# Optimization experiments

Hardware: AMD Instinct MI355X
Metric: run time of the kernel (lower is better)

Reference implementation:

```python
import jax, jax.numpy as jnp
import numpy as np

INF = 1.0e10


def _embed(x, W1, b1, W2, b2):
    # TemplateAngleEmbedder: Linear -> GELU -> Linear
    return jax.nn.gelu(x @ W1 + b1) @ W2 + b2


def setup_inputs() -> dict:
    key = jax.random.key(0)
    ks = jax.random.split(key, 12)
    B, N, K = 2, 768, 30
    d_pair, d_msa, relpos_k = 128, 256, 32
    num_bins = 2 * relpos_k + 1  # 65
    s = 0.02
    # valid rigid frames: random rotations via QR (det fixed to +1) + translations
    A = jax.random.normal(ks[0], (B, N, 3, 3), dtype=jnp.float32)
    Q, _ = jnp.linalg.qr(A)
    Q = Q * jnp.sign(jnp.linalg.det(Q))[..., None, None]
    t = jax.random.normal(ks[1], (B, N, 3), dtype=jnp.float32) * 10.0
    frames = (jnp.zeros((B, N, 4, 4), dtype=jnp.float32)
              .at[..., :3, :3].set(Q)
              .at[..., :3, 3].set(t)
              .at[..., 3, 3].set(1.0))
    residue_index = jnp.tile(jnp.arange(N, dtype=jnp.int32)[None], (B, 1))
    return {
        'tf': jax.random.normal(ks[2], (B, N, 1), dtype=jnp.float32),
        'residue_index': residue_index,
        'true_frame_tensor': frames,
        'seq_mask': jnp.ones((B, N), dtype=jnp.float32),
        'W_tf': jax.random.normal(ks[3], (1, d_msa), dtype=jnp.float32) * s,
        'b_tf': jnp.zeros((d_msa,), dtype=jnp.float32),
        'Wa1': jax.random.normal(ks[4], (5, d_pair), dtype=jnp.float32) * s,
        'ba1': jnp.zeros((d_pair,), dtype=jnp.float32),
        'Wa2': jax.random.normal(ks[5], (d_pair, d_pair), dtype=jnp.float32) * s,
        'ba2': jnp.zeros((d_pair,), dtype=jnp.float32),
        'Wd1': jax.random.normal(ks[6], (3, d_pair), dtype=jnp.float32) * s,
        'bd1': jnp.zeros((d_pair,), dtype=jnp.float32),
        'Wd2': jax.random.normal(ks[7], (d_pair, d_pair), dtype=jnp.float32) * s,
        'bd2': jnp.zeros((d_pair,), dtype=jnp.float32),
        'W_rp': jax.random.normal(ks[8], (num_bins, d_pair), dtype=jnp.float32) * s,
        'b_rp': jnp.zeros((d_pair,), dtype=jnp.float32),
        'topk': 30,
    }


def _pair_features(true_frame_tensor, residue_index, seq_mask, topk):
    # get_pair_info: pairwise dist + masked topk KNN + gather + frame decompose
    B, N = residue_index.shape
    R = true_frame_tensor[..., :3, :3]          # [B,N,3,3]
    t = true_frame_tensor[..., :3, 3]           # [B,N,3]
    xyz = t[:, None, :, :] - t[:, :, None, :]   # [B,i,j,3] = t_j - t_i
    dist = jnp.linalg.norm(xyz, axis=-1)        # [B,N,N]
    eye = jnp.eye(N, dtype=bool)[None]          # [1,N,N]
    smask = seq_mask.astype(bool)
    pair_mask = smask[:, None, :] & smask[:, :, None]
    rel = residue_index[:, None, :] - residue_index[:, :, None]
    connect = jnp.abs(rel) == 1
    d4topk = jnp.where(eye, INF, dist)
    d4topk = jnp.where(pair_mask, d4topk, INF)
    d4topk = jnp.where(connect, -INF, d4topk)
    _, idx = jax.lax.top_k(-d4topk, topk)       # k smallest -> [B,N,K]
    topk_dist = jnp.take_along_axis(dist, idx, axis=-1)          # [B,N,K]
    knn_mask = jnp.take_along_axis(pair_mask & ~eye, idx, axis=-1)
    # gather neighbor frames and decompose into frame i's local coordinates:
    # t_rel = R_i^T (t_j - t_i)
    bidx = jnp.arange(B)[:, None, None]
    tj = t[bidx, idx]                            # [B,N,K,3]
    t_rel = jnp.einsum('bnxy,bnkx->bnky', R, tj - t[:, :, None, :])
    d = topk_dist[..., None]
    direct_angle = jnp.where(d > 0, t_rel / jnp.where(d > 0, d, 1.0), 0.0)
    eye_g = jnp.take_along_axis(jnp.broadcast_to(eye, (B, N, N)), idx, axis=-1)
    conn_g = jnp.take_along_axis(connect, idx, axis=-1)
    f32 = topk_dist.dtype
    ang_in = jnp.concatenate([eye_g[..., None].astype(f32),
                              conn_g[..., None].astype(f32),
                              direct_angle], axis=-1)            # [B,N,K,5]
    dst_in = jnp.concatenate([eye_g[..., None].astype(f32),
                              conn_g[..., None].astype(f32),
                              topk_dist[..., None]], axis=-1)    # [B,N,K,3]
    return ang_in, dst_in, knn_mask


def reference(tf, residue_index, true_frame_tensor, seq_mask,
              W_tf, b_tf, Wa1, ba1, Wa2, ba2, Wd1, bd1, Wd2, bd2,
              W_rp, b_rp, topk):
    relpos_k = (W_rp.shape[0] - 1) // 2
    # pair info computed under no_grad in the original
    ang_in, dst_in, _ = jax.lax.stop_gradient(
        _pair_features(true_frame_tensor, residue_index, seq_mask, topk))
    # tf is replaced by ones in the original forward
    ones_tf = jnp.ones_like(tf[..., :1])
    s = ones_tf @ W_tf + b_tf                                   # [B,N,d_msa]
    pair_rep_angle = _embed(ang_in, Wa1, ba1, Wa2, ba2)         # [B,N,K,d_pair]
    pair_rep_dist = _embed(dst_in, Wd1, bd1, Wd2, bd2)          # [B,N,K,d_pair]
    # relpos embedding (use_chain_relative=False)
    rp = residue_index[:, :, None] - residue_index[:, None, :]
    rp = jnp.clip(rp, -relpos_k, relpos_k) + relpos_k
    oh = jax.nn.one_hot(rp, W_rp.shape[0], dtype=W_rp.dtype)    # [B,N,N,65]
    relpos_emb = oh @ W_rp + b_rp                               # [B,N,N,d_pair]
    return (s, pair_rep_angle, pair_rep_dist, relpos_emb)
```

## Files before the change

kernel.cpp:

```cpp
#include <hip/hip_runtime.h>

typedef unsigned short u16;
typedef unsigned int   u32;
typedef unsigned long long u64;

typedef __attribute__((ext_vector_type(8))) short  short8;
typedef __attribute__((ext_vector_type(4))) float  floatx4;

__device__ __forceinline__ u16 f2bf(float f) {
    u32 u = __float_as_uint(f);
    u32 r = (u + 0x7FFFu + ((u >> 16) & 1u)) >> 16;
    return (u16)r;
}
__device__ __forceinline__ float bfu2f(u16 u) {
    union { u32 i; float f; } v; v.i = ((u32)u) << 16; return v.f;
}

constexpr int N     = 768;
constexpr int TOPK  = 30;
constexpr long OFF_ANG = 393216;
constexpr long OFF_DST = 6291456;
constexpr long OFF_RP  = 12189696;

__device__ __forceinline__ float dist_f32(float dx, float dy, float dz) {
    float s = __fadd_rn(__fadd_rn(__fmul_rn(dx, dx), __fmul_rn(dy, dy)), __fmul_rn(dz, dz));
    return __fsqrt_rn(s);
}

__global__ __launch_bounds__(256) void topk_relpos_kernel(
    const float* __restrict__ frames, const int* __restrict__ resi,
    const float* __restrict__ smask, float* __restrict__ feat,
    const float* __restrict__ W_rp, const float* __restrict__ b_rp,
    float* __restrict__ out)
{
    __shared__ __align__(16) char smem_raw[65 * 128 * 4 + N * 4];
    int tid = threadIdx.x;

    if (blockIdx.x < 384) {
        float* s_t = (float*)smem_raw;
        float* s_m = s_t + N * 3;
        int*   s_r = (int*)(s_m + N);

        int r0  = blockIdx.x * 4;
        int b   = r0 / N;
        for (int j = tid; j < N; j += 256) {
            s_r[j] = resi[b * N + j];
            s_m[j] = smask[b * N + j];
            long fb = (long)(b * N + j) * 16;
            s_t[j * 3 + 0] = frames[fb + 0 * 4 + 3];
            s_t[j * 3 + 1] = frames[fb + 1 * 4 + 3];
            s_t[j * 3 + 2] = frames[fb + 2 * 4 + 3];
        }
        __syncthreads();

        int wave = tid >> 6, lane = tid & 63;
        int r = r0 + wave;
        int i = r - b * N;
        float ti0 = s_t[i * 3], ti1 = s_t[i * 3 + 1], ti2 = s_t[i * 3 + 2];
        float mi = s_m[i];
        int   ri = s_r[i];

        u64 keys[12];
#pragma unroll
        for (int c = 0; c < 12; c++) {
            int j = lane + 64 * c;
            float dx = __fadd_rn(s_t[j * 3 + 0], -ti0);
            float dy = __fadd_rn(s_t[j * 3 + 1], -ti1);
            float dz = __fadd_rn(s_t[j * 3 + 2], -ti2);
            float dist = dist_f32(dx, dy, dz);
            int rd = s_r[j] - ri;
            bool conn = (rd == 1) || (rd == -1);
            bool bad  = (j == i) || (mi == 0.f) || (s_m[j] == 0.f);
            float d4 = conn ? -1e10f : (bad ? 1e10f : dist);
            u32 u = __float_as_uint(d4);
            u32 su = (u >> 31) ? ~u : (u | 0x80000000u);
            keys[c] = ((u64)su << 32) | (u32)j;
        }

        int my_j = 0;
        for (int k = 0; k < TOPK; k++) {
            u64 m = keys[0];
#pragma unroll
            for (int c = 1; c < 12; c++) m = m < keys[c] ? m : keys[c];
#pragma unroll
            for (int off = 32; off >= 1; off >>= 1) {
                u32 lo = (u32)m, hi = (u32)(m >> 32);
                u32 lo2 = __shfl_xor(lo, off);
                u32 hi2 = __shfl_xor(hi, off);
                u64 o = ((u64)hi2 << 32) | lo2;
                m = m < o ? m : o;
            }
#pragma unroll
            for (int c = 0; c < 12; c++) keys[c] = (keys[c] == m) ? ~0ull : keys[c];
            if (lane == k) my_j = (int)(m & 0xffffffffu);
        }

        if (lane < TOPK) {
            int j = my_j;
            float dx = __fadd_rn(s_t[j * 3 + 0], -ti0);
            float dy = __fadd_rn(s_t[j * 3 + 1], -ti1);
            float dz = __fadd_rn(s_t[j * 3 + 2], -ti2);
            float dist = dist_f32(dx, dy, dz);
            long fb = (long)(b * N + i) * 16;
            float R00 = frames[fb + 0], R01 = frames[fb + 1], R02 = frames[fb + 2];
            float R10 = frames[fb + 4], R11 = frames[fb + 5], R12 = frames[fb + 6];
            float R20 = frames[fb + 8], R21 = frames[fb + 9], R22 = frames[fb + 10];
            float t0 = R00 * dx + R10 * dy + R20 * dz;
            float t1 = R01 * dx + R11 * dy + R21 * dz;
            float t2 = R02 * dx + R12 * dy + R22 * dz;
            float a0 = dist > 0.f ? t0 / dist : 0.f;
            float a1 = dist > 0.f ? t1 / dist : 0.f;
            float a2 = dist > 0.f ? t2 / dist : 0.f;
            int rd = s_r[j] - ri;
            float conn = ((rd == 1) || (rd == -1)) ? 1.f : 0.f;
            float eye  = (j == i) ? 1.f : 0.f;
            long base = ((long)r * TOPK + lane) * 8;
            feat[base + 0] = eye; feat[base + 1] = conn;
            feat[base + 2] = a0;  feat[base + 3] = a1; feat[base + 4] = a2;
            feat[base + 5] = eye; feat[base + 6] = conn; feat[base + 7] = dist;
        }
    } else {
        float* T   = (float*)smem_raw;
        int*   s_r = (int*)(T + 65 * 128);

        int blk = blockIdx.x - 384;
        int b   = blk >= 576;

        for (int e = tid; e < 65 * 128; e += 256) T[e] = W_rp[e] + b_rp[e & 127];
        for (int j = tid; j < N; j += 256) s_r[j] = resi[b * N + j];
        __syncthreads();

        long vbase   = (long)blk << 15;
        int  rowbase = (blk - b * 576) << 10;
        floatx4* dst = (floatx4*)(out + OFF_RP) + vbase;

#pragma unroll 4
        for (int it = 0; it < 128; ++it) {
            int lv  = (it << 8) + tid;
            unsigned lrow = (unsigned)(rowbase + (lv >> 5));
            int seg = lv & 31;
            unsigned i = lrow / 768u;
            unsigned j = lrow - i * 768u;
            int d = s_r[i] - s_r[j];
            d = d < -32 ? -32 : (d > 32 ? 32 : d);
            dst[lv] = ((const floatx4*)(T + (unsigned)(d + 32) * 128))[seg];
        }
    }
}

template<int NF, int FOFF>
__device__ __forceinline__ void embed_body(
    int blk, const float* __restrict__ feat,
    const float* __restrict__ W1, const float* __restrict__ b1,
    const float* __restrict__ W2, const float* __restrict__ b2,
    float* __restrict__ out,
    u16* s_w2h, u16* s_w2l, float* s_w1, float* s_b1, float* s_b2)
{
    int tid = threadIdx.x;
    for (int e = tid; e < 128 * 128; e += 256) {
        int kk = e >> 7, nn = e & 127;
        float w  = W2[e];
        u16 hi = f2bf(w);
        float lo = __fadd_rn(w, -bfu2f(hi));
        s_w2h[nn * 136 + kk] = hi;
        s_w2l[nn * 136 + kk] = f2bf(lo);
    }
    for (int e = tid; e < NF * 128; e += 256) s_w1[e] = W1[e];
    if (tid < 128) { s_b1[tid] = b1[tid]; s_b2[tid] = b2[tid]; }
    __syncthreads();

    int wave = tid >> 6, lane = tid & 63;
    int m = lane & 15, q = lane >> 4;
    int row0 = blk * 64 + wave * 16;
    int row  = row0 + m;

    float f[NF];
#pragma unroll
    for (int t = 0; t < NF; t++) f[t] = feat[(long)row * 8 + FOFF + t];

    floatx4 acc[8];
#pragma unroll
    for (int nt = 0; nt < 8; nt++) acc[nt] = (floatx4){0.f, 0.f, 0.f, 0.f};

#pragma unroll
    for (int s = 0; s < 4; s++) {
        short8 ahi, alo;
#pragma unroll
        for (int jj = 0; jj < 8; jj++) {
            int kk = 32 * s + 8 * q + jj;
            float h = s_b1[kk];
#pragma unroll
            for (int t = 0; t < NF; t++) h += f[t] * s_w1[t * 128 + kk];
            float u  = 0.7978845608028654f * (h + 0.044715f * h * h * h);
            float e2 = __expf(-2.f * fabsf(u));
            float th = (1.f - e2) / (1.f + e2);
            th = u < 0.f ? -th : th;
            float g = 0.5f * h * (1.f + th);
            u16 ghi = f2bf(g);
            float glo = __fadd_rn(g, -bfu2f(ghi));
            ahi[jj] = (short)ghi;
            alo[jj] = (short)f2bf(glo);
        }
#pragma unroll
        for (int nt = 0; nt < 8; nt++) {
            int boff = (nt * 16 + m) * 136 + 32 * s + 8 * q;
            short8 bh = *(const short8*)&s_w2h[boff];
            short8 bl = *(const short8*)&s_w2l[boff];
            acc[nt] = __builtin_amdgcn_mfma_f32_16x16x32_bf16(ahi, bh, acc[nt], 0, 0, 0);
            acc[nt] = __builtin_amdgcn_mfma_f32_16x16x32_bf16(alo, bh, acc[nt], 0, 0, 0);
            acc[nt] = __builtin_amdgcn_mfma_f32_16x16x32_bf16(ahi, bl, acc[nt], 0, 0, 0);
        }
    }

#pragma unroll
    for (int nt = 0; nt < 8; nt++) {
#pragma unroll
        for (int rg = 0; rg < 4; rg++) {
            int rr = row0 + q * 4 + rg;
            int cc = nt * 16 + m;
            out[(long)rr * 128 + cc] = acc[nt][rg] + s_b2[cc];
        }
    }
}

__global__ __launch_bounds__(256) void fused_embed_s_kernel(
    const float* __restrict__ feat,
    const float* __restrict__ Wa1, const float* __restrict__ ba1,
    const float* __restrict__ Wa2, const float* __restrict__ ba2,
    const float* __restrict__ Wd1, const float* __restrict__ bd1,
    const float* __restrict__ Wd2, const float* __restrict__ bd2,
    const float* __restrict__ W_tf, const float* __restrict__ b_tf,
    float* __restrict__ out)
{
    __shared__ __align__(16) u16 s_w2h[128 * 136];
    __shared__ __align__(16) u16 s_w2l[128 * 136];
    __shared__ float s_w1[5 * 128];
    __shared__ float s_b1[128];
    __shared__ float s_b2[128];
    unsigned bx = blockIdx.x;
    if (bx < 720) {
        embed_body<5, 0>(bx, feat, Wa1, ba1, Wa2, ba2, out + OFF_ANG,
                         s_w2h, s_w2l, s_w1, s_b1, s_b2);
    } else if (bx < 1440) {
        embed_body<3, 5>(bx - 720, feat, Wd1, bd1, Wd2, bd2, out + OFF_DST,
                         s_w2h, s_w2l, s_w1, s_b1, s_b2);
    } else {
        int gid = (bx - 1440) * 256 + threadIdx.x;
        int c0  = (gid * 4) & 255;
        floatx4 o;
        o.x = W_tf[c0 + 0] + b_tf[c0 + 0];
        o.y = W_tf[c0 + 1] + b_tf[c0 + 1];
        o.z = W_tf[c0 + 2] + b_tf[c0 + 2];
        o.w = W_tf[c0 + 3] + b_tf[c0 + 3];
        *((floatx4*)out + gid) = o;
    }
}

extern "C" void kernel_launch(void* const* d_in, const int* in_sizes, int n_in,
                              void* d_out, int out_size, void* d_ws, size_t ws_size,
                              hipStream_t stream) {
    const int*   resi   = (const int*)d_in[1];
    const float* frames = (const float*)d_in[2];
    const float* smask  = (const float*)d_in[3];
    const float* W_tf   = (const float*)d_in[4];
    const float* b_tf   = (const float*)d_in[5];
    const float* Wa1    = (const float*)d_in[6];
    const float* ba1    = (const float*)d_in[7];
    const float* Wa2    = (const float*)d_in[8];
    const float* ba2    = (const float*)d_in[9];
    const float* Wd1    = (const float*)d_in[10];
    const float* bd1    = (const float*)d_in[11];
    const float* Wd2    = (const float*)d_in[12];
    const float* bd2    = (const float*)d_in[13];
    const float* W_rp   = (const float*)d_in[14];
    const float* b_rp   = (const float*)d_in[15];
    float* out  = (float*)d_out;
    float* feat = (float*)d_ws;

    hipLaunchKernelGGL(topk_relpos_kernel, dim3(1536), dim3(256), 0, stream,
                       frames, resi, smask, feat, W_rp, b_rp, out);
    hipLaunchKernelGGL(fused_embed_s_kernel, dim3(1824), dim3(256), 0, stream,
                       feat, Wa1, ba1, Wa2, ba2, Wd1, bd1, Wd2, bd2,
                       W_tf, b_tf, out);
}
```

Baseline: 701.0 us.

## Split top-k into its own kernel and co-schedule relpos with embedding MLPs

The top-k feature kernel now runs alone with 384 blocks. The relpos broadcast moves into a second mega kernel next to the angle and distance embed MLPs, so the bandwidth-bound relpos writes can overlap with MFMA-bound embedding work instead of overlapping with top-k. Each embed block now handles three 64-row tiles, which amortizes the W2 bf16 hi/lo split into LDS across more rows, and W2 is read with float4 loads. The costs are a larger shared allocation (about 73 KB) for every block in the mega kernel, which may cut occupancy for the relpos blocks, and a top-k kernel with few blocks that may underfill the GPU.

Result: slower. 747.5 us (+6.6%).

```diff
diff --git a/kernel.cpp b/kernel.cpp
--- a/kernel.cpp
+++ b/kernel.cpp
@@ -27,103 +27,199 @@
     return __fsqrt_rn(s);
 }
 
-__global__ __launch_bounds__(256) void topk_relpos_kernel(
+__global__ __launch_bounds__(256) void topk_feat_kernel(
     const float* __restrict__ frames, const int* __restrict__ resi,
-    const float* __restrict__ smask, float* __restrict__ feat,
+    const float* __restrict__ smask, float* __restrict__ feat)
+{
+    __shared__ float s_t[N * 3];
+    __shared__ float s_m[N];
+    __shared__ int   s_r[N];
+    int tid = threadIdx.x;
+    int r0  = blockIdx.x * 4;
+    int b   = r0 / N;
+    for (int j = tid; j < N; j += 256) {
+        s_r[j] = resi[b * N + j];
+        s_m[j] = smask[b * N + j];
+        long fb = (long)(b * N + j) * 16;
+        s_t[j * 3 + 0] = frames[fb + 0 * 4 + 3];
+        s_t[j * 3 + 1] = frames[fb + 1 * 4 + 3];
+        s_t[j * 3 + 2] = frames[fb + 2 * 4 + 3];
+    }
+    __syncthreads();
+
+    int wave = tid >> 6, lane = tid & 63;
+    int r = r0 + wave;
+    int i = r - b * N;
+    float ti0 = s_t[i * 3], ti1 = s_t[i * 3 + 1], ti2 = s_t[i * 3 + 2];
+    float mi = s_m[i];
+    int   ri = s_r[i];
+
+    u64 keys[12];
+#pragma unroll
+    for (int c = 0; c < 12; c++) {
+        int j = lane + 64 * c;
+        float dx = __fadd_rn(s_t[j * 3 + 0], -ti0);
+        float dy = __fadd_rn(s_t[j * 3 + 1], -ti1);
+        float dz = __fadd_rn(s_t[j * 3 + 2], -ti2);
+        float dist = dist_f32(dx, dy, dz);
+        int rd = s_r[j] - ri;
+        bool conn = (rd == 1) || (rd == -1);
+        bool bad  = (j == i) || (mi == 0.f) || (s_m[j] == 0.f);
+        float d4 = conn ? -1e10f : (bad ? 1e10f : dist);
+        u32 u = __float_as_uint(d4);
+        u32 su = (u >> 31) ? ~u : (u | 0x80000000u);
+        keys[c] = ((u64)su << 32) | (u32)j;
+    }
+
+    int my_j = 0;
+    for (int k = 0; k < TOPK; k++) {
+        u64 m = keys[0];
+#pragma unroll
+        for (int c = 1; c < 12; c++) m = m < keys[c] ? m : keys[c];
+#pragma unroll
+        for (int off = 32; off >= 1; off >>= 1) {
+            u32 lo = (u32)m, hi = (u32)(m >> 32);
+            u32 lo2 = __shfl_xor(lo, off);
+            u32 hi2 = __shfl_xor(hi, off);
+            u64 o = ((u64)hi2 << 32) | lo2;
+            m = m < o ? m : o;
+        }
+#pragma unroll
+        for (int c = 0; c < 12; c++) keys[c] = (keys[c] == m) ? ~0ull : keys[c];
+        if (lane == k) my_j = (int)(m & 0xffffffffu);
+    }
+
+    if (lane < TOPK) {
+        int j = my_j;
+        float dx = __fadd_rn(s_t[j * 3 + 0], -ti0);
+        float dy = __fadd_rn(s_t[j * 3 + 1], -ti1);
+        float dz = __fadd_rn(s_t[j * 3 + 2], -ti2);
+        float dist = dist_f32(dx, dy, dz);
+        long fb = (long)(b * N + i) * 16;
+        float R00 = frames[fb + 0], R01 = frames[fb + 1], R02 = frames[fb + 2];
+        float R10 = frames[fb + 4], R11 = frames[fb + 5], R12 = frames[fb + 6];
+        float R20 = frames[fb + 8], R21 = frames[fb + 9], R22 = frames[fb + 10];
+        float t0 = R00 * dx + R10 * dy + R20 * dz;
+        float t1 = R01 * dx + R11 * dy + R21 * dz;
+        float t2 = R02 * dx + R12 * dy + R22 * dz;
+        float a0 = dist > 0.f ? t0 / dist : 0.f;
+        float a1 = dist > 0.f ? t1 / dist : 0.f;
+        float a2 = dist > 0.f ? t2 / dist : 0.f;
+        int rd = s_r[j] - ri;
+        float conn = ((rd == 1) || (rd == -1)) ? 1.f : 0.f;
+        float eye  = (j == i) ? 1.f : 0.f;
+        long base = ((long)r * TOPK + lane) * 8;
+        feat[base + 0] = eye; feat[base + 1] = conn;
+        feat[base + 2] = a0;  feat[base + 3] = a1; feat[base + 4] = a2;
+        feat[base + 5] = eye; feat[base + 6] = conn; feat[base + 7] = dist;
+    }
+}
+
+template<int NF, int FOFF>
+__device__ __forceinline__ void embed_body3(
+    int blk0, const float* __restrict__ feat,
+    const float* __restrict__ W1, const float* __restrict__ b1,
+    const float* __restrict__ W2, const float* __restrict__ b2,
+    float* __restrict__ out,
+    u16* s_w2h, u16* s_w2l, float* s_w1, float* s_b1, float* s_b2)
+{
+    int tid = threadIdx.x;
+    for (int e4 = tid; e4 < 4096; e4 += 256) {
+        floatx4 w4 = ((const floatx4*)W2)[e4];
+        int e  = e4 * 4;
+        int kk = e >> 7, nn0 = e & 127;
+#pragma unroll
+        for (int x = 0; x < 4; x++) {
+            float w  = w4[x];
+            u16 hi = f2bf(w);
+            float lo = __fadd_rn(w, -bfu2f(hi));
+            s_w2h[(nn0 + x) * 136 + kk] = hi;
+            s_w2l[(nn0 + x) * 136 + kk] = f2bf(lo);
+        }
+    }
+    for (int e = tid; e < NF * 128; e += 256) s_w1[e] = W1[e];
+    if (tid < 128) { s_b1[tid] = b1[tid]; s_b2[tid] = b2[tid]; }
+    __syncthreads();
+
+    int wave = tid >> 6, lane = tid & 63;
+    int m = lane & 15, q = lane >> 4;
+
+#pragma unroll
+    for (int tt = 0; tt < 3; tt++) {
+        int blk  = blk0 + 240 * tt;
+        int row0 = blk * 64 + wave * 16;
+        int row  = row0 + m;
+
+        float f[NF];
+#pragma unroll
+        for (int t = 0; t < NF; t++) f[t] = feat[(long)row * 8 + FOFF + t];
+
+        floatx4 acc[8];
+#pragma unroll
+        for (int nt = 0; nt < 8; nt++) acc[nt] = (floatx4){0.f, 0.f, 0.f, 0.f};
+
+#pragma unroll
+        for (int s = 0; s < 4; s++) {
+            short8 ahi, alo;
+#pragma unroll
+            for (int jj = 0; jj < 8; jj++) {
+                int kk = 32 * s + 8 * q + jj;
+                float h = s_b1[kk];
+#pragma unroll
+                for (int t = 0; t < NF; t++) h += f[t] * s_w1[t * 128 + kk];
+                float u  = 0.7978845608028654f * (h + 0.044715f * h * h * h);
+                float e2 = __expf(-2.f * fabsf(u));
+                float th = (1.f - e2) / (1.f + e2);
+                th = u < 0.f ? -th : th;
+                float g = 0.5f * h * (1.f + th);
+                u16 ghi = f2bf(g);
+                float glo = __fadd_rn(g, -bfu2f(ghi));
+                ahi[jj] = (short)ghi;
+                alo[jj] = (short)f2bf(glo);
+            }
+#pragma unroll
+            for (int nt = 0; nt < 8; nt++) {
+                int boff = (nt * 16 + m) * 136 + 32 * s + 8 * q;
+                short8 bh = *(const short8*)&s_w2h[boff];
+                short8 bl = *(const short8*)&s_w2l[boff];
+                acc[nt] = __builtin_amdgcn_mfma_f32_16x16x32_bf16(ahi, bh, acc[nt], 0, 0, 0);
+                acc[nt] = __builtin_amdgcn_mfma_f32_16x16x32_bf16(alo, bh, acc[nt], 0, 0, 0);
+                acc[nt] = __builtin_amdgcn_mfma_f32_16x16x32_bf16(ahi, bl, acc[nt], 0, 0, 0);
+            }
+        }
+
+#pragma unroll
+        for (int nt = 0; nt < 8; nt++) {
+#pragma unroll
+            for (int rg = 0; rg < 4; rg++) {
+                int rr = row0 + q * 4 + rg;
+                int cc = nt * 16 + m;
+                out[(long)rr * 128 + cc] = acc[nt][rg] + s_b2[cc];
+            }
+        }
+    }
+}
+
+__global__ __launch_bounds__(256) void mega_kernel(
+    const int* __restrict__ resi,
     const float* __restrict__ W_rp, const float* __restrict__ b_rp,
+    const float* __restrict__ feat,
+    const float* __restrict__ Wa1, const float* __restrict__ ba1,
+    const float* __restrict__ Wa2, const float* __restrict__ ba2,
+    const float* __restrict__ Wd1, const float* __restrict__ bd1,
+    const float* __restrict__ Wd2, const float* __restrict__ bd2,
+    const float* __restrict__ W_tf, const float* __restrict__ b_tf,
     float* __restrict__ out)
 {
-    __shared__ __align__(16) char smem_raw[65 * 128 * 4 + N * 4];
+    __shared__ __align__(16) char smem_raw[73216];
     int tid = threadIdx.x;
-
-    if (blockIdx.x < 384) {
-        float* s_t = (float*)smem_raw;
-        float* s_m = s_t + N * 3;
-        int*   s_r = (int*)(s_m + N);
-
-        int r0  = blockIdx.x * 4;
-        int b   = r0 / N;
-        for (int j = tid; j < N; j += 256) {
-            s_r[j] = resi[b * N + j];
-            s_m[j] = smask[b * N + j];
-            long fb = (long)(b * N + j) * 16;
-            s_t[j * 3 + 0] = frames[fb + 0 * 4 + 3];
-            s_t[j * 3 + 1] = frames[fb + 1 * 4 + 3];
-            s_t[j * 3 + 2] = frames[fb + 2 * 4 + 3];
-        }
-        __syncthreads();
-
-        int wave = tid >> 6, lane = tid & 63;
-        int r = r0 + wave;
-        int i = r - b * N;
-        float ti0 = s_t[i * 3], ti1 = s_t[i * 3 + 1], ti2 = s_t[i * 3 + 2];
-        float mi = s_m[i];
-        int   ri = s_r[i];
-
-        u64 keys[12];
-#pragma unroll
-        for (int c = 0; c < 12; c++) {
-            int j = lane + 64 * c;
-            float dx = __fadd_rn(s_t[j * 3 + 0], -ti0);
-            float dy = __fadd_rn(s_t[j * 3 + 1], -ti1);
-            float dz = __fadd_rn(s_t[j * 3 + 2], -ti2);
-            float dist = dist_f32(dx, dy, dz);
-            int rd = s_r[j] - ri;
-            bool conn = (rd == 1) || (rd == -1);
-            bool bad  = (j == i) || (mi == 0.f) || (s_m[j] == 0.f);
-            float d4 = conn ? -1e10f : (bad ? 1e10f : dist);
-            u32 u = __float_as_uint(d4);
-            u32 su = (u >> 31) ? ~u : (u | 0x80000000u);
-            keys[c] = ((u64)su << 32) | (u32)j;
-        }
-
-        int my_j = 0;
-        for (int k = 0; k < TOPK; k++) {
-            u64 m = keys[0];
-#pragma unroll
-            for (int c = 1; c < 12; c++) m = m < keys[c] ? m : keys[c];
-#pragma unroll
-            for (int off = 32; off >= 1; off >>= 1) {
-                u32 lo = (u32)m, hi = (u32)(m >> 32);
-                u32 lo2 = __shfl_xor(lo, off);
-                u32 hi2 = __shfl_xor(hi, off);
-                u64 o = ((u64)hi2 << 32) | lo2;
-                m = m < o ? m : o;
-            }
-#pragma unroll
-            for (int c = 0; c < 12; c++) keys[c] = (keys[c] == m) ? ~0ull : keys[c];
-            if (lane == k) my_j = (int)(m & 0xffffffffu);
-        }
-
-        if (lane < TOPK) {
-            int j = my_j;
-            float dx = __fadd_rn(s_t[j * 3 + 0], -ti0);
-            float dy = __fadd_rn(s_t[j * 3 + 1], -ti1);
-            float dz = __fadd_rn(s_t[j * 3 + 2], -ti2);
-            float dist = dist_f32(dx, dy, dz);
-            long fb = (long)(b * N + i) * 16;
-            float R00 = frames[fb + 0], R01 = frames[fb + 1], R02 = frames[fb + 2];
-            float R10 = frames[fb + 4], R11 = frames[fb + 5], R12 = frames[fb + 6];
-            float R20 = frames[fb + 8], R21 = frames[fb + 9], R22 = frames[fb + 10];
-            float t0 = R00 * dx + R10 * dy + R20 * dz;
-            float t1 = R01 * dx + R11 * dy + R21 * dz;
-            float t2 = R02 * dx + R12 * dy + R22 * dz;
-            float a0 = dist > 0.f ? t0 / dist : 0.f;
-            float a1 = dist > 0.f ? t1 / dist : 0.f;
-            float a2 = dist > 0.f ? t2 / dist : 0.f;
-            int rd = s_r[j] - ri;
-            float conn = ((rd == 1) || (rd == -1)) ? 1.f : 0.f;
-            float eye  = (j == i) ? 1.f : 0.f;
-            long base = ((long)r * TOPK + lane) * 8;
-            feat[base + 0] = eye; feat[base + 1] = conn;
-            feat[base + 2] = a0;  feat[base + 3] = a1; feat[base + 4] = a2;
-            feat[base + 5] = eye; feat[base + 6] = conn; feat[base + 7] = dist;
-        }
-    } else {
+    unsigned bx = blockIdx.x;
+
+    if (bx < 1152) {
         float* T   = (float*)smem_raw;
         int*   s_r = (int*)(T + 65 * 128);
 
-        int blk = blockIdx.x - 384;
+        int blk = bx;
         int b   = blk >= 576;
 
         for (int e = tid; e < 65 * 128; e += 256) T[e] = W_rp[e] + b_rp[e & 127];
@@ -145,107 +241,22 @@
             d = d < -32 ? -32 : (d > 32 ? 32 : d);
             dst[lv] = ((const floatx4*)(T + (unsigned)(d + 32) * 128))[seg];
         }
-    }
-}
-
-template<int NF, int FOFF>
-__device__ __forceinline__ void embed_body(
-    int blk, const float* __restrict__ feat,
-    const float* __restrict__ W1, const float* __restrict__ b1,
-    const float* __restrict__ W2, const float* __restrict__ b2,
-    float* __restrict__ out,
-    u16* s_w2h, u16* s_w2l, float* s_w1, float* s_b1, float* s_b2)
-{
-    int tid = threadIdx.x;
-    for (int e = tid; e < 128 * 128; e += 256) {
-        int kk = e >> 7, nn = e & 127;
-        float w  = W2[e];
-        u16 hi = f2bf(w);
-        float lo = __fadd_rn(w, -bfu2f(hi));
-        s_w2h[nn * 136 + kk] = hi;
-        s_w2l[nn * 136 + kk] = f2bf(lo);
-    }
-    for (int e = tid; e < NF * 128; e += 256) s_w1[e] = W1[e];
-    if (tid < 128) { s_b1[tid] = b1[tid]; s_b2[tid] = b2[tid]; }
-    __syncthreads();
-
-    int wave = tid >> 6, lane = tid & 63;
-    int m = lane & 15, q = lane >> 4;
-    int row0 = blk * 64 + wave * 16;
-    int row  = row0 + m;
-
-    float f[NF];
-#pragma unroll
-    for (int t = 0; t < NF; t++) f[t] = feat[(long)row * 8 + FOFF + t];
-
-    floatx4 acc[8];
-#pragma unroll
-    for (int nt = 0; nt < 8; nt++) acc[nt] = (floatx4){0.f, 0.f, 0.f, 0.f};
-
-#pragma unroll
-    for (int s = 0; s < 4; s++) {
-        short8 ahi, alo;
-#pragma unroll
-        for (int jj = 0; jj < 8; jj++) {
-            int kk = 32 * s + 8 * q + jj;
-            float h = s_b1[kk];
-#pragma unroll
-            for (int t = 0; t < NF; t++) h += f[t] * s_w1[t * 128 + kk];
-            float u  = 0.7978845608028654f * (h + 0.044715f * h * h * h);
-            float e2 = __expf(-2.f * fabsf(u));
-            float th = (1.f - e2) / (1.f + e2);
-            th = u < 0.f ? -th : th;
-            float g = 0.5f * h * (1.f + th);
-            u16 ghi = f2bf(g);
-            float glo = __fadd_rn(g, -bfu2f(ghi));
-            ahi[jj] = (short)ghi;
-            alo[jj] = (short)f2bf(glo);
-        }
-#pragma unroll
-        for (int nt = 0; nt < 8; nt++) {
-            int boff = (nt * 16 + m) * 136 + 32 * s + 8 * q;
-            short8 bh = *(const short8*)&s_w2h[boff];
-            short8 bl = *(const short8*)&s_w2l[boff];
-            acc[nt] = __builtin_amdgcn_mfma_f32_16x16x32_bf16(ahi, bh, acc[nt], 0, 0, 0);
-            acc[nt] = __builtin_amdgcn_mfma_f32_16x16x32_bf16(alo, bh, acc[nt], 0, 0, 0);
-            acc[nt] = __builtin_amdgcn_mfma_f32_16x16x32_bf16(ahi, bl, acc[nt], 0, 0, 0);
-        }
-    }
-
-#pragma unroll
-    for (int nt = 0; nt < 8; nt++) {
-#pragma unroll
-        for (int rg = 0; rg < 4; rg++) {
-            int rr = row0 + q * 4 + rg;
-            int cc = nt * 16 + m;
-            out[(long)rr * 128 + cc] = acc[nt][rg] + s_b2[cc];
-        }
-    }
-}
-
-__global__ __launch_bounds__(256) void fused_embed_s_kernel(
-    const float* __restrict__ feat,
-    const float* __restrict__ Wa1, const float* __restrict__ ba1,
-    const float* __restrict__ Wa2, const float* __restrict__ ba2,
-    const float* __restrict__ Wd1, const float* __restrict__ bd1,
-    const float* __restrict__ Wd2, const float* __restrict__ bd2,
-    const float* __restrict__ W_tf, const float* __restrict__ b_tf,
-    float* __restrict__ out)
-{
-    __shared__ __align__(16) u16 s_w2h[128 * 136];
-    __shared__ __align__(16) u16 s_w2l[128 * 136];
-    __shared__ float s_w1[5 * 128];
-    __shared__ float s_b1[128];
-    __shared__ float s_b2[128];
-    unsigned bx = blockIdx.x;
-    if (bx < 720) {
-        embed_body<5, 0>(bx, feat, Wa1, ba1, Wa2, ba2, out + OFF_ANG,
-                         s_w2h, s_w2l, s_w1, s_b1, s_b2);
-    } else if (bx < 1440) {
-        embed_body<3, 5>(bx - 720, feat, Wd1, bd1, Wd2, bd2, out + OFF_DST,
-                         s_w2h, s_w2l, s_w1, s_b1, s_b2);
+    } else if (bx < 1632) {
+        u16*   s_w2h = (u16*)smem_raw;
+        u16*   s_w2l = (u16*)(smem_raw + 34816);
+        float* s_w1  = (float*)(smem_raw + 69632);
+        float* s_b1  = (float*)(smem_raw + 72192);
+        float* s_b2  = (float*)(smem_raw + 72704);
+        unsigned eb = bx - 1152;
+        if (eb < 240) {
+            embed_body3<5, 0>(eb, feat, Wa1, ba1, Wa2, ba2, out + OFF_ANG,
+                              s_w2h, s_w2l, s_w1, s_b1, s_b2);
+        } else {
+            embed_body3<3, 5>(eb - 240, feat, Wd1, bd1, Wd2, bd2, out + OFF_DST,
+                              s_w2h, s_w2l, s_w1, s_b1, s_b2);
+        }
     } else {
-        int gid = (bx - 1440) * 256 + threadIdx.x;
+        int gid = (bx - 1632) * 256 + tid;
         int c0  = (gid * 4) & 255;
         floatx4 o;
         o.x = W_tf[c0 + 0] + b_tf[c0 + 0];
@@ -277,9 +288,10 @@
     float* out  = (float*)d_out;
     float* feat = (float*)d_ws;
 
-    hipLaunchKernelGGL(topk_relpos_kernel, dim3(1536), dim3(256), 0, stream,
-                       frames, resi, smask, feat, W_rp, b_rp, out);
-    hipLaunchKernelGGL(fused_embed_s_kernel, dim3(1824), dim3(256), 0, stream,
-                       feat, Wa1, ba1, Wa2, ba2, Wd1, bd1, Wd2, bd2,
+    hipLaunchKernelGGL(topk_feat_kernel, dim3(384), dim3(256), 0, stream,
+                       frames, resi, smask, feat);
+    hipLaunchKernelGGL(mega_kernel, dim3(2016), dim3(256), 0, stream,
+                       resi, W_rp, b_rp, feat,
+                       Wa1, ba1, Wa2, ba2, Wd1, bd1, Wd2, bd2,
                        W_tf, b_tf, out);
 }
```
